# Kernel tuning notes

Measured on AMD Instinct MI355X. Metric: run time of the kernel, lower is better.

Reference implementation:

```python
import jax, jax.numpy as jnp
import numpy as np

N, E, H, B = 100000, 1600000, 64, 256
EPS = 1e-5


def ln(x, g, b):
    mu = jnp.mean(x, axis=-1, keepdims=True)
    var = jnp.mean((x - mu) ** 2, axis=-1, keepdims=True)
    return (x - mu) * jax.lax.rsqrt(var + EPS) * g + b


def gelu(x):
    # torch nn.GELU default is exact (erf) gelu
    return jax.nn.gelu(x, approximate=False)


def setup_inputs() -> dict:
    key = jax.random.key(0)
    ks = iter(jax.random.split(key, 64))
    nk = lambda: next(ks)
    s = 0.1
    p = {}
    p["x"] = jax.random.normal(nk(), (N, 2), jnp.float32)
    p["edge_attr"] = jax.random.normal(nk(), (E, 2), jnp.float32)
    # node_embed: Linear(2,H) LN GELU Linear(H,H) LN GELU (dropout = eval no-op)
    p["ne_w1"] = jax.random.normal(nk(), (2, H), jnp.float32) * s
    p["ne_b1"] = jnp.zeros((H,), jnp.float32)
    p["ne_g1"] = jnp.ones((H,), jnp.float32)
    p["ne_be1"] = jnp.zeros((H,), jnp.float32)
    p["ne_w2"] = jax.random.normal(nk(), (H, H), jnp.float32) * s
    p["ne_b2"] = jnp.zeros((H,), jnp.float32)
    p["ne_g2"] = jnp.ones((H,), jnp.float32)
    p["ne_be2"] = jnp.zeros((H,), jnp.float32)
    # 3 TrackConv layers: message MLP Linear(H+2,H)+LN, conv output LN, and outer per-layer LN
    p["conv_w"] = jax.random.normal(nk(), (3, H + 2, H), jnp.float32) * s
    p["conv_b"] = jnp.zeros((3, H), jnp.float32)
    p["conv_mg"] = jnp.ones((3, H), jnp.float32)
    p["conv_mb"] = jnp.zeros((3, H), jnp.float32)
    p["conv_ng"] = jnp.ones((3, H), jnp.float32)
    p["conv_nb"] = jnp.zeros((3, H), jnp.float32)
    p["out_ng"] = jnp.ones((3, H), jnp.float32)
    p["out_nb"] = jnp.zeros((3, H), jnp.float32)
    # head MLP: Linear(H,H)+LN+ReLU, Linear(H,H//2)+LN+ReLU, Linear(H//2,1)
    p["m_w1"] = jax.random.normal(nk(), (H, H), jnp.float32) * s
    p["m_b1"] = jnp.zeros((H,), jnp.float32)
    p["m_g1"] = jnp.ones((H,), jnp.float32)
    p["m_be1"] = jnp.zeros((H,), jnp.float32)
    p["m_w2"] = jax.random.normal(nk(), (H, H // 2), jnp.float32) * s
    p["m_b2"] = jnp.zeros((H // 2,), jnp.float32)
    p["m_g2"] = jnp.ones((H // 2,), jnp.float32)
    p["m_be2"] = jnp.zeros((H // 2,), jnp.float32)
    p["m_w3"] = jax.random.normal(nk(), (H // 2, 1), jnp.float32) * s
    p["m_b3"] = jnp.zeros((1,), jnp.float32)
    p["edge_index"] = jax.random.randint(nk(), (2, E), 0, N, dtype=jnp.int32)
    p["batch"] = jnp.sort(jax.random.randint(nk(), (N,), 0, B, dtype=jnp.int32))
    return p


def reference(x, edge_attr,
              ne_w1, ne_b1, ne_g1, ne_be1, ne_w2, ne_b2, ne_g2, ne_be2,
              conv_w, conv_b, conv_mg, conv_mb, conv_ng, conv_nb, out_ng, out_nb,
              m_w1, m_b1, m_g1, m_be1, m_w2, m_b2, m_g2, m_be2, m_w3, m_b3,
              edge_index, batch):
    # node embedding (dropout in eval = identity)
    h = gelu(ln(x @ ne_w1 + ne_b1, ne_g1, ne_be1))
    h = gelu(ln(h @ ne_w2 + ne_b2, ne_g2, ne_be2))
    src, dst = edge_index[0], edge_index[1]  # PyG: message from src (x_j), aggregate at dst
    deg = jax.ops.segment_sum(jnp.ones((E,), h.dtype), dst, num_segments=N)
    deg = jnp.maximum(deg, 1.0)[:, None]
    for l in range(3):
        msg_in = jnp.concatenate([h[src], edge_attr], axis=-1)  # [E, H+2]
        msg = gelu(ln(msg_in @ conv_w[l] + conv_b[l], conv_mg[l], conv_mb[l]))  # [E, H]
        agg = jax.ops.segment_sum(msg, dst, num_segments=N) / deg  # mean aggregate
        conv_out = ln(agg + h, conv_ng[l], conv_nb[l])  # TrackConv: norm(out + residual)
        h = h + ln(conv_out, out_ng[l], out_nb[l])  # outer norm + residual
    # global mean pool over graphs
    cnt = jnp.maximum(jax.ops.segment_sum(jnp.ones((N,), h.dtype), batch, num_segments=B), 1.0)[:, None]
    g = jax.ops.segment_sum(h, batch, num_segments=B) / cnt  # [B, H]
    g = jax.nn.relu(ln(g @ m_w1 + m_b1, m_g1, m_be1))
    g = jax.nn.relu(ln(g @ m_w2 + m_b2, m_g2, m_be2))
    return g @ m_w3 + m_b3  # [B, 1]
```

## Files before the change

kernel.cpp:

```cpp
#include <hip/hip_runtime.h>
#include <math.h>


typedef __attribute__((ext_vector_type(8))) short bfrag;
typedef __attribute__((ext_vector_type(4))) float ffrag;

template <int CTRL>
__device__ __forceinline__ float dpp_mov(float v) {
  return __int_as_float(
      __builtin_amdgcn_update_dpp(0, __float_as_int(v), CTRL, 0xF, 0xF, true));
}

__device__ __forceinline__ float rsum16(float v) {
  v += dpp_mov<0x128>(v);
  v += dpp_mov<0x124>(v);
  v += dpp_mov<0x122>(v);
  v += dpp_mov<0x121>(v);
  return v;
}

__device__ __forceinline__ float wave_sum64(float v) {
  v = rsum16(v);
  v += __shfl_xor(v, 16, 64);
  v += __shfl_xor(v, 32, 64);
  return v;
}

__device__ __forceinline__ float ln_apply(float t, float g, float b) {
  float s1 = wave_sum64(t);
  float s2 = wave_sum64(t * t);
  float mu = s1 * 0.015625f;
  float var = fmaf(-mu, mu, s2 * 0.015625f);
  return (t - mu) * rsqrtf(var + 1e-5f) * g + b;
}

__device__ __forceinline__ float erf_fast(float x) {
  float ax = fabsf(x);
  float p = fmaf(fmaf(fmaf(fmaf(0.078108f, ax, 0.000972f), ax, 0.230389f),
                      ax, 0.278393f), ax, 1.0f);
  p = p * p;
  p = p * p;
  float r = __builtin_amdgcn_rcpf(p);
  return copysignf(1.0f - r, x);
}

__device__ __forceinline__ float gelu_exact(float v) {
  float half = 0.5f * v;
  return fmaf(half, erf_fast(v * 0.70710678118654752440f), half);
}

__device__ __forceinline__ float lane_bcast(float v, int k) {
  return __uint_as_float(__builtin_amdgcn_readlane(__float_as_uint(v), k));
}

__device__ __forceinline__ short f2bf(float f) {
  union { float f; unsigned u; } v; v.f = f;
  unsigned r = v.u + 0x7fffu + ((v.u >> 16) & 1u);
  return (short)(r >> 16);
}

__global__ __launch_bounds__(256) void k_init1(
    const float* __restrict__ conv_w, ushort* __restrict__ wt,
    const int* __restrict__ ei, int* __restrict__ csr,
    int ne, int oHist) {
  const int bid = blockIdx.x;
  const int tid = threadIdx.x;
  if (bid < oHist) {
    const int i = bid * 256 + tid;
    const int k = i % 96, f = (i / 96) % 64, l = i / (96 * 64);
    const float v = (k < 66) ? conv_w[(size_t)l * 66 * 64 + k * 64 + f] : 0.0f;
    wt[i] = (ushort)f2bf(v);
    return;
  }
  const int i = (bid - oHist) * 256 + tid;
  if (i < ne) atomicAdd(&csr[__builtin_nontemporal_load(ei + ne + i)], 1);
}

__global__ __launch_bounds__(1024) void k_scan_fast(int* __restrict__ buf, int n) {
  __shared__ int wsum[16];
  const int tid = threadIdx.x, lane = tid & 63, w = tid >> 6;
  const int chunk = (((n + 1023) / 1024) + 3) & ~3;
  const int a = min(tid * chunk, n), b = min(a + chunk, n);
  const bool full = (a + chunk <= n);
  int s = 0;
  if (full) {
    const int4* p4 = (const int4*)(buf + a);
#pragma unroll 4
    for (int i = 0; i < chunk / 4; i++) {
      int4 v = p4[i];
      s += v.x + v.y + v.z + v.w;
    }
  } else {
    for (int i = a; i < b; i++) s += buf[i];
  }
  int inc = s;
#pragma unroll
  for (int sh = 1; sh < 64; sh <<= 1) {
    int t = __shfl_up(inc, sh, 64);
    if (lane >= sh) inc += t;
  }
  if (lane == 63) wsum[w] = inc;
  __syncthreads();
  int wb = 0;
  for (int j = 0; j < w; j++) wb += wsum[j];
  int excl = wb + inc - s;
  if (full) {
    int4* p4 = (int4*)(buf + a);
#pragma unroll 4
    for (int i = 0; i < chunk / 4; i++) {
      int4 v = p4[i];
      int4 o;
      o.x = excl; excl += v.x;
      o.y = excl; excl += v.y;
      o.z = excl; excl += v.z;
      o.w = excl; excl += v.w;
      p4[i] = o;
    }
  } else {
    for (int i = a; i < b; i++) { int v = buf[i]; buf[i] = excl; excl += v; }
  }
}

__global__ __launch_bounds__(256) void k_combo(
    const int* __restrict__ ei, const float* __restrict__ ea,
    int* __restrict__ cursor, int4* __restrict__ edata,
    const float* __restrict__ x,
    const float* __restrict__ w1, const float* __restrict__ b1,
    const float* __restrict__ g1, const float* __restrict__ be1,
    const float* __restrict__ w2, const float* __restrict__ b2,
    const float* __restrict__ g2, const float* __restrict__ be2,
    float* __restrict__ h, ushort* __restrict__ hb,
    int n_nodes, int ne, int nOrd, int embWaves, float roleScale) {
  const int bid = blockIdx.x;
  const int tid = threadIdx.x;
  const int sub = bid & 31;
  if (sub < 24) {
    const int role = bid & 7;
    const int ord = (bid >> 5) * 3 + (sub >> 3);
    const int lo = (int)((long long)ord * ne / nOrd);
    const int hi = (int)((long long)(ord + 1) * ne / nOrd);
    for (int i = lo + tid; i < hi; i += 256) {
      const int d = __builtin_nontemporal_load(ei + ne + i);
      const int rd = min(7, (int)((float)d * roleScale));
      if (rd == role) {
        const int s = __builtin_nontemporal_load(ei + i);
        const unsigned long long eau =
            __builtin_nontemporal_load((const unsigned long long*)ea + i);
        const float e0 = __uint_as_float((unsigned)eau);
        const float e1 = __uint_as_float((unsigned)(eau >> 32));
        const unsigned pk = (unsigned)(ushort)f2bf(e0) |
                            ((unsigned)(ushort)f2bf(e1) << 16);
        const int pos = atomicAdd(&cursor[d], 1);
        edata[pos] = make_int4(s, (int)pk, d, 0);
      }
    }
    return;
  }
  const int lane = tid & 63;
  const int eblk = (bid >> 5) * 8 + (sub - 24);
  const int wid = (eblk * 256 + tid) >> 6;
  const int nw = embWaves;
  float wc[64];
#pragma unroll
  for (int k = 0; k < 64; k++) wc[k] = w2[k * 64 + lane];
  const float w1a = w1[lane], w1b = w1[64 + lane];
  const float vb1 = b1[lane], vg1 = g1[lane], vbe1 = be1[lane];
  const float vb2 = b2[lane], vg2 = g2[lane], vbe2 = be2[lane];
  for (int n = wid; n < n_nodes; n += nw) {
    const float x0 = x[2 * n], x1 = x[2 * n + 1];
    float t = fmaf(x0, w1a, fmaf(x1, w1b, vb1));
    t = gelu_exact(ln_apply(t, vg1, vbe1));
    float a0 = vb2, a1 = 0.f, a2 = 0.f, a3 = 0.f;
#pragma unroll
    for (int k = 0; k < 64; k += 4) {
      a0 = fmaf(lane_bcast(t, k + 0), wc[k + 0], a0);
      a1 = fmaf(lane_bcast(t, k + 1), wc[k + 1], a1);
      a2 = fmaf(lane_bcast(t, k + 2), wc[k + 2], a2);
      a3 = fmaf(lane_bcast(t, k + 3), wc[k + 3], a3);
    }
    float acc = (a0 + a1) + (a2 + a3);
    acc = gelu_exact(ln_apply(acc, vg2, vbe2));
    __builtin_nontemporal_store(acc, h + (size_t)n * 64 + lane);
    __builtin_nontemporal_store((ushort)f2bf(acc),
                                hb + (size_t)n * 64 + lane);
  }
}

__global__ __launch_bounds__(256, 3) void k_edge_packed(
    const ushort* __restrict__ hb_in, float* __restrict__ agg,
    const int4* __restrict__ edata, const ushort* __restrict__ wt,
    const float* __restrict__ bias, const float* __restrict__ mg,
    const float* __restrict__ mb, int nchunks, int ne) {
  __shared__ __align__(16) ushort lwt[64 * 96];
  {
    const uint4* s = (const uint4*)wt;
    uint4* d = (uint4*)lwt;
    for (int i = threadIdx.x; i < 768; i += 256) d[i] = s[i];
  }
  __syncthreads();

  const int lane = threadIdx.x & 63;
  const int grp = lane >> 4, col = lane & 15;
  const int wid = (blockIdx.x * blockDim.x + threadIdx.x) >> 6;
  const int nw = (gridDim.x * blockDim.x) >> 6;

  float vb[4], vg[4], vbb[4];
#pragma unroll
  for (int t = 0; t < 4; t++) {
    const int f = t * 16 + col;
    vb[t] = bias[f]; vg[t] = mg[f]; vbb[t] = mb[f];
  }

  int c = wid;
  if (c >= nchunks) return;
  int4 e = edata[min(16 * c + col, ne - 1)];
  const ushort* hp0 = hb_in + (size_t)e.x * 64 + grp * 8;
  bfrag A0 = *(const bfrag*)(hp0);
  bfrag A1 = *(const bfrag*)(hp0 + 32);

  for (;;) {
    const int rem = min(16, ne - 16 * c);
    const int cn = c + nw;
    const bool more = cn < nchunks;
    const int nslot = more ? min(16 * cn + col, ne - 1) : min(16 * c + col, ne - 1);
    const int4 en = edata[nslot];

    bfrag A2 = {0, 0, 0, 0, 0, 0, 0, 0};
    if (grp == 0) {
      A2[0] = (short)(e.y & 0xffff);
      A2[1] = (short)((unsigned)e.y >> 16);
    }

    ffrag acc[4];
#pragma unroll
    for (int t = 0; t < 4; t++) { ffrag cc = {vb[t], vb[t], vb[t], vb[t]}; acc[t] = cc; }
#pragma unroll
    for (int t = 0; t < 4; t++) {
      const bfrag B = *(const bfrag*)(lwt + (t * 16 + col) * 96 + grp * 8);
      acc[t] = __builtin_amdgcn_mfma_f32_16x16x32_bf16(A0, B, acc[t], 0, 0, 0);
    }
#pragma unroll
    for (int t = 0; t < 4; t++) {
      const bfrag B = *(const bfrag*)(lwt + (t * 16 + col) * 96 + 32 + grp * 8);
      acc[t] = __builtin_amdgcn_mfma_f32_16x16x32_bf16(A1, B, acc[t], 0, 0, 0);
    }
#pragma unroll
    for (int t = 0; t < 4; t++) {
      const bfrag B = *(const bfrag*)(lwt + (t * 16 + col) * 96 + 64 + grp * 8);
      acc[t] = __builtin_amdgcn_mfma_f32_16x16x32_bf16(A2, B, acc[t], 0, 0, 0);
    }

    const ushort* hq = hb_in + (size_t)en.x * 64 + grp * 8;
    const bfrag N0 = *(const bfrag*)(hq);
    const bfrag N1 = *(const bfrag*)(hq + 32);

    float sx[4], sq[4];
#pragma unroll
    for (int r = 0; r < 4; r++) {
      float s = (acc[0][r] + acc[1][r]) + (acc[2][r] + acc[3][r]);
      float q = fmaf(acc[0][r], acc[0][r], fmaf(acc[1][r], acc[1][r],
                fmaf(acc[2][r], acc[2][r], acc[3][r] * acc[3][r])));
      sx[r] = s; sq[r] = q;
    }
#pragma unroll
    for (int r = 0; r < 4; r++) sx[r] = rsum16(sx[r]);
#pragma unroll
    for (int r = 0; r < 4; r++) sq[r] = rsum16(sq[r]);
    float iv[4], mi[4];
#pragma unroll
    for (int r = 0; r < 4; r++) {
      const float mu = sx[r] * 0.015625f;
      const float var = fmaf(-mu, mu, sq[r] * 0.015625f);
      iv[r] = rsqrtf(var + 1e-5f);
      mi[r] = -mu * iv[r];
    }

#pragma unroll
    for (int t = 0; t < 4; t++) {
#pragma unroll
      for (int r = 0; r < 4; r++) {
        const float z = fmaf(acc[t][r], iv[r], mi[r]);
        acc[t][r] = gelu_exact(fmaf(z, vg[t], vbb[t]));
      }
    }

    const int prev = __shfl_up(e.z, 1, 64);
    const unsigned long long bal = __ballot((col > 0) && (e.z != prev));
    const unsigned bm = (unsigned)bal & 0xFFFEu;

    int s0 = 0;
    while (s0 < rem) {
      const unsigned rest = bm >> (s0 + 1);
      int s1 = rest ? (s0 + 1 + __builtin_ctz(rest)) : 16;
      if (s1 > rem) s1 = rem;
      const int dseg = __builtin_amdgcn_readlane(e.z, s0);
#pragma unroll
      for (int t = 0; t < 4; t++) {
        float rs = 0.f;
#pragma unroll
        for (int r = 0; r < 4; r++) {
          const int row = grp * 4 + r;
          const float w = (row >= s0 && row < s1) ? 1.0f : 0.0f;
          rs = fmaf(acc[t][r], w, rs);
        }
        rs += __shfl_xor(rs, 16, 64);
        rs += __shfl_xor(rs, 32, 64);
        if (lane < 16)
          atomicAdd(&agg[(size_t)dseg * 64 + t * 16 + lane], rs);
      }
      s0 = s1;
    }

    if (!more) break;
    c = cn; e = en; A0 = N0; A1 = N1;
  }
}

__global__ void k_node_update(float* __restrict__ h, ushort* __restrict__ hb,
                              float* __restrict__ agg, const int* __restrict__ ends,
                              const float* __restrict__ ng, const float* __restrict__ nb,
                              const float* __restrict__ og, const float* __restrict__ ob,
                              int n_nodes, int writeHb) {
  const int lane = threadIdx.x & 63;
  const int n = (blockIdx.x * blockDim.x + threadIdx.x) >> 6;
  if (n >= n_nodes) return;
  int start, end;
  if (n == 0) { start = 0; end = ends[0]; }
  else { const int2 se = *(const int2*)(ends + n - 1); start = se.x; end = se.y; }
  const float dg = fmaxf((float)(end - start), 1.0f);
  const float hv = h[(size_t)n * 64 + lane];
  const float a = agg[(size_t)n * 64 + lane] / dg + hv;
  if (writeHb) agg[(size_t)n * 64 + lane] = 0.0f;
  const float c = ln_apply(a, ng[lane], nb[lane]);
  const float o = ln_apply(c, og[lane], ob[lane]);
  const float outv = hv + o;
  h[(size_t)n * 64 + lane] = outv;
  if (writeHb) hb[(size_t)n * 64 + lane] = (ushort)f2bf(outv);
}

__global__ void k_pool_seg(const float* __restrict__ h, const int* __restrict__ batch,
                           float* __restrict__ g, float* __restrict__ cnt,
                           int n_nodes, int chunk) {
  const int lane = threadIdx.x & 63;
  const int wid = (blockIdx.x * blockDim.x + threadIdx.x) >> 6;
  const int n0 = wid * chunk;
  if (n0 >= n_nodes) return;
  const int n1 = min(n0 + chunk, n_nodes);
  int cur = batch[n0], c = 0;
  float acc = 0.f;
  for (int n = n0; n < n1; n++) {
    const int b = batch[n];
    if (b != cur) {
      atomicAdd(&g[(size_t)cur * 64 + lane], acc);
      if (lane == 0) atomicAdd(&cnt[cur], (float)c);
      acc = 0.f; c = 0; cur = b;
    }
    acc += h[(size_t)n * 64 + lane];
    c++;
  }
  atomicAdd(&g[(size_t)cur * 64 + lane], acc);
  if (lane == 0) atomicAdd(&cnt[cur], (float)c);
}

__global__ void k_head(const float* __restrict__ g, const float* __restrict__ cnt,
                       const float* __restrict__ w1, const float* __restrict__ b1,
                       const float* __restrict__ g1, const float* __restrict__ be1,
                       const float* __restrict__ w2, const float* __restrict__ b2,
                       const float* __restrict__ g2, const float* __restrict__ be2,
                       const float* __restrict__ w3, const float* __restrict__ b3,
                       float* __restrict__ out, int nb_) {
  const int lane = threadIdx.x & 63;
  const int row = (blockIdx.x * blockDim.x + threadIdx.x) >> 6;
  if (row >= nb_) return;
  const float c = fmaxf(cnt[row], 1.0f);
  const float gv = g[row * 64 + lane] / c;
  float a0 = b1[lane], a1 = 0.f, a2 = 0.f, a3 = 0.f;
#pragma unroll
  for (int k = 0; k < 64; k += 4) {
    a0 = fmaf(lane_bcast(gv, k + 0), w1[(k + 0) * 64 + lane], a0);
    a1 = fmaf(lane_bcast(gv, k + 1), w1[(k + 1) * 64 + lane], a1);
    a2 = fmaf(lane_bcast(gv, k + 2), w1[(k + 2) * 64 + lane], a2);
    a3 = fmaf(lane_bcast(gv, k + 3), w1[(k + 3) * 64 + lane], a3);
  }
  float t = (a0 + a1) + (a2 + a3);
  t = fmaxf(ln_apply(t, g1[lane], be1[lane]), 0.0f);

  const int j = lane & 31;
  float c0 = b2[j], c1 = 0.f, c2 = 0.f, c3 = 0.f;
#pragma unroll
  for (int k = 0; k < 64; k += 4) {
    c0 = fmaf(lane_bcast(t, k + 0), w2[(k + 0) * 32 + j], c0);
    c1 = fmaf(lane_bcast(t, k + 1), w2[(k + 1) * 32 + j], c1);
    c2 = fmaf(lane_bcast(t, k + 2), w2[(k + 2) * 32 + j], c2);
    c3 = fmaf(lane_bcast(t, k + 3), w2[(k + 3) * 32 + j], c3);
  }
  float t2 = (c0 + c1) + (c2 + c3);
  t2 = fmaxf(ln_apply(t2, g2[j], be2[j]), 0.0f);
  const float p = t2 * w3[j];
  const float s = wave_sum64(p) * 0.5f;
  if (lane == 0) out[row] = s + b3[0];
}

extern "C" void kernel_launch(void* const* d_in, const int* in_sizes, int n_in,
                              void* d_out, int out_size, void* d_ws, size_t ws_size,
                              hipStream_t stream) {
  const float* x      = (const float*)d_in[0];
  const float* ea     = (const float*)d_in[1];
  const float* ne_w1  = (const float*)d_in[2];
  const float* ne_b1  = (const float*)d_in[3];
  const float* ne_g1  = (const float*)d_in[4];
  const float* ne_be1 = (const float*)d_in[5];
  const float* ne_w2  = (const float*)d_in[6];
  const float* ne_b2  = (const float*)d_in[7];
  const float* ne_g2  = (const float*)d_in[8];
  const float* ne_be2 = (const float*)d_in[9];
  const float* conv_w = (const float*)d_in[10];
  const float* conv_b = (const float*)d_in[11];
  const float* conv_mg= (const float*)d_in[12];
  const float* conv_mb= (const float*)d_in[13];
  const float* conv_ng= (const float*)d_in[14];
  const float* conv_nb= (const float*)d_in[15];
  const float* out_ng = (const float*)d_in[16];
  const float* out_nb = (const float*)d_in[17];
  const float* m_w1   = (const float*)d_in[18];
  const float* m_b1   = (const float*)d_in[19];
  const float* m_g1   = (const float*)d_in[20];
  const float* m_be1  = (const float*)d_in[21];
  const float* m_w2   = (const float*)d_in[22];
  const float* m_b2   = (const float*)d_in[23];
  const float* m_g2   = (const float*)d_in[24];
  const float* m_be2  = (const float*)d_in[25];
  const float* m_w3   = (const float*)d_in[26];
  const float* m_b3   = (const float*)d_in[27];
  const int*   eidx   = (const int*)d_in[28];
  const int*   batch  = (const int*)d_in[29];
  float* outp = (float*)d_out;

  const int NN = in_sizes[29];
  const int NE = in_sizes[1] / 2;
  const int NB = out_size;
  const int NCH = (NE + 15) / 16;

  char* wsb = (char*)d_ws;
  float*  h    = (float*)wsb;
  ushort* hb   = (ushort*)(h + (size_t)NN * 64);
  int4*   edata= (int4*)((char*)hb + ((size_t)NN * 128 + 15) / 16 * 16);
  ushort* wt   = (ushort*)(edata + NE);
  float*  gbuf = (float*)(wt + 3 * 64 * 96);
  float*  cnt  = gbuf + (size_t)NB * 64;
  int*    csr  = (int*)(cnt + NB);
  float*  agg  = (float*)((char*)(csr + NN) +
                          (((size_t)(uintptr_t)(csr + NN) & 15) ? 16 - ((size_t)(uintptr_t)(csr + NN) & 15) : 0));

  const dim3 blk(256);

  const size_t zbytes = (char*)(agg + (size_t)NN * 64) - (char*)gbuf;
  hipMemsetAsync(gbuf, 0, zbytes, stream);

  const int nPrep = (3 * 64 * 96) / 256;
  const int nHist = (NE + 255) / 256;
  k_init1<<<nPrep + nHist, blk, 0, stream>>>(conv_w, wt, eidx, csr, NE, nPrep);

  k_scan_fast<<<1, 1024, 0, stream>>>(csr, NN);

  const int ngroups = 261;
  const int nOrd = ngroups * 3;
  const int nEmb = ngroups * 8;
  k_combo<<<ngroups * 32, blk, 0, stream>>>(
      eidx, ea, csr, edata, x,
      ne_w1, ne_b1, ne_g1, ne_be1, ne_w2, ne_b2, ne_g2, ne_be2,
      h, hb, NN, NE, nOrd, nEmb * 4, 8.0f / (float)NN);

  for (int l = 0; l < 3; l++) {
    k_edge_packed<<<4096, blk, 0, stream>>>(
        hb, agg, edata, wt + (size_t)l * 64 * 96,
        conv_b + l * 64, conv_mg + l * 64, conv_mb + l * 64, NCH, NE);
    k_node_update<<<(NN * 64 + 255) / 256, blk, 0, stream>>>(
        h, hb, agg, csr, conv_ng + l * 64, conv_nb + l * 64,
        out_ng + l * 64, out_nb + l * 64, NN, (l < 2) ? 1 : 0);
  }

  {
    const int chunk = 32;
    const int nwaves = (NN + chunk - 1) / chunk;
    const int nblocks = (nwaves * 64 + 255) / 256;
    k_pool_seg<<<nblocks, blk, 0, stream>>>(h, batch, gbuf, cnt, NN, chunk);
  }
  k_head<<<(NB + 3) / 4, blk, 0, stream>>>(gbuf, cnt, m_w1, m_b1, m_g1, m_be1,
                                           m_w2, m_b2, m_g2, m_be2, m_w3, m_b3,
                                           outp, NB);
}
```

Measured before the change: 744.6 us.

## Bucket edges by destination block and aggregate messages in LDS before storing

Edges are now sorted only into buckets of 131 destination nodes rather than fully by destination. Each record is packed into an int2 holding the source index, the local destination offset and the bf16 edge attributes. The edge kernel runs one block per bucket and accumulates messages with LDS atomics into a padded local tile, then writes the tile to global agg with plain stores. This removes global float atomics, the per-node agg zeroing, and half of the edge-record bandwidth. In exchange, per-bucket work can be uneven, LDS atomic contention rises, and LDS use per block grows, which may lower occupancy.

```diff
diff --git a/kernel.cpp b/kernel.cpp
--- a/kernel.cpp
+++ b/kernel.cpp
@@ -4,6 +4,11 @@
 
 typedef __attribute__((ext_vector_type(8))) short bfrag;
 typedef __attribute__((ext_vector_type(4))) float ffrag;
+typedef __attribute__((ext_vector_type(4))) float f32x4;
+
+#define WBUK 131
+#define MAGW 4196609267u
+#define LSTR 68
 
 template <int CTRL>
 __device__ __forceinline__ float dpp_mov(float v) {
@@ -76,7 +81,9 @@
   if (i < ne) atomicAdd(&csr[__builtin_nontemporal_load(ei + ne + i)], 1);
 }
 
-__global__ __launch_bounds__(1024) void k_scan_fast(int* __restrict__ buf, int n) {
+__global__ __launch_bounds__(1024) void k_scan_fast(int* __restrict__ buf,
+                                                    int* __restrict__ bcur,
+                                                    int n, int nbuck) {
   __shared__ int wsum[16];
   const int tid = threadIdx.x, lane = tid & 63, w = tid >> 6;
   const int chunk = (((n + 1023) / 1024) + 3) & ~3;
@@ -119,18 +126,26 @@
   } else {
     for (int i = a; i < b; i++) { int v = buf[i]; buf[i] = excl; excl += v; }
   }
+  __syncthreads();
+  if (tid == 0) {
+    int tot = 0;
+#pragma unroll
+    for (int j = 0; j < 16; j++) tot += wsum[j];
+    buf[n] = tot;
+  }
+  for (int bq = tid; bq < nbuck; bq += 1024) bcur[bq] = buf[min(bq * WBUK, n)];
 }
 
 __global__ __launch_bounds__(256) void k_combo(
     const int* __restrict__ ei, const float* __restrict__ ea,
-    int* __restrict__ cursor, int4* __restrict__ edata,
+    int* __restrict__ bcur, int2* __restrict__ edata,
     const float* __restrict__ x,
     const float* __restrict__ w1, const float* __restrict__ b1,
     const float* __restrict__ g1, const float* __restrict__ be1,
     const float* __restrict__ w2, const float* __restrict__ b2,
     const float* __restrict__ g2, const float* __restrict__ be2,
     float* __restrict__ h, ushort* __restrict__ hb,
-    int n_nodes, int ne, int nOrd, int embWaves, float roleScale) {
+    int n_nodes, int ne, int nOrd, int embWaves) {
   const int bid = blockIdx.x;
   const int tid = threadIdx.x;
   const int sub = bid & 31;
@@ -141,8 +156,8 @@
     const int hi = (int)((long long)(ord + 1) * ne / nOrd);
     for (int i = lo + tid; i < hi; i += 256) {
       const int d = __builtin_nontemporal_load(ei + ne + i);
-      const int rd = min(7, (int)((float)d * roleScale));
-      if (rd == role) {
+      const unsigned bq = __umulhi((unsigned)d, MAGW) >> 7;
+      if ((int)(bq & 7u) == role) {
         const int s = __builtin_nontemporal_load(ei + i);
         const unsigned long long eau =
             __builtin_nontemporal_load((const unsigned long long*)ea + i);
@@ -150,8 +165,9 @@
         const float e1 = __uint_as_float((unsigned)(eau >> 32));
         const unsigned pk = (unsigned)(ushort)f2bf(e0) |
                             ((unsigned)(ushort)f2bf(e1) << 16);
-        const int pos = atomicAdd(&cursor[d], 1);
-        edata[pos] = make_int4(s, (int)pk, d, 0);
+        const int dloc = d - (int)bq * WBUK;
+        const int pos = atomicAdd(&bcur[bq], 1);
+        edata[pos] = make_int2(s | (dloc << 20), (int)pk);
       }
     }
     return;
@@ -186,23 +202,31 @@
   }
 }
 
-__global__ __launch_bounds__(256, 3) void k_edge_packed(
+__global__ __launch_bounds__(256, 3) void k_edge_lds(
     const ushort* __restrict__ hb_in, float* __restrict__ agg,
-    const int4* __restrict__ edata, const ushort* __restrict__ wt,
+    const int2* __restrict__ edata, const int* __restrict__ csr,
+    const ushort* __restrict__ wt,
     const float* __restrict__ bias, const float* __restrict__ mg,
-    const float* __restrict__ mb, int nchunks, int ne) {
+    const float* __restrict__ mb, int nn) {
   __shared__ __align__(16) ushort lwt[64 * 96];
+  __shared__ __align__(16) float lagg[WBUK * LSTR];
   {
     const uint4* s = (const uint4*)wt;
     uint4* d = (uint4*)lwt;
     for (int i = threadIdx.x; i < 768; i += 256) d[i] = s[i];
-  }
+    f32x4* z = (f32x4*)lagg;
+    const f32x4 zz = {0.f, 0.f, 0.f, 0.f};
+    for (int i = threadIdx.x; i < (WBUK * LSTR) / 4; i += 256) z[i] = zz;
+  }
+  const int bq = blockIdx.x;
+  const int nlo = bq * WBUK;
+  const int nhi = min(nlo + WBUK, nn);
+  const int lo = csr[nlo], hi = csr[nhi];
   __syncthreads();
 
   const int lane = threadIdx.x & 63;
+  const int wv = threadIdx.x >> 6;
   const int grp = lane >> 4, col = lane & 15;
-  const int wid = (blockIdx.x * blockDim.x + threadIdx.x) >> 6;
-  const int nw = (gridDim.x * blockDim.x) >> 6;
 
   float vb[4], vg[4], vbb[4];
 #pragma unroll
@@ -211,126 +235,122 @@
     vb[t] = bias[f]; vg[t] = mg[f]; vbb[t] = mb[f];
   }
 
-  int c = wid;
-  if (c >= nchunks) return;
-  int4 e = edata[min(16 * c + col, ne - 1)];
-  const ushort* hp0 = hb_in + (size_t)e.x * 64 + grp * 8;
-  bfrag A0 = *(const bfrag*)(hp0);
-  bfrag A1 = *(const bfrag*)(hp0 + 32);
-
-  for (;;) {
-    const int rem = min(16, ne - 16 * c);
-    const int cn = c + nw;
-    const bool more = cn < nchunks;
-    const int nslot = more ? min(16 * cn + col, ne - 1) : min(16 * c + col, ne - 1);
-    const int4 en = edata[nslot];
-
-    bfrag A2 = {0, 0, 0, 0, 0, 0, 0, 0};
-    if (grp == 0) {
-      A2[0] = (short)(e.y & 0xffff);
-      A2[1] = (short)((unsigned)e.y >> 16);
+  const int nch = (hi - lo + 15) >> 4;
+  int c = wv;
+  if (c < nch) {
+    int slot = min(lo + 16 * c + col, hi - 1);
+    int2 e = edata[slot];
+    const ushort* hp0 = hb_in + (size_t)(e.x & 0xFFFFF) * 64 + grp * 8;
+    bfrag A0 = *(const bfrag*)(hp0);
+    bfrag A1 = *(const bfrag*)(hp0 + 32);
+
+    for (;;) {
+      const int rem = min(16, hi - lo - 16 * c);
+      const int cn = c + 4;
+      const bool more = cn < nch;
+      const int nslot = more ? min(lo + 16 * cn + col, hi - 1) : slot;
+      const int2 en = edata[nslot];
+
+      bfrag A2 = {0, 0, 0, 0, 0, 0, 0, 0};
+      if (grp == 0) {
+        A2[0] = (short)(e.y & 0xffff);
+        A2[1] = (short)((unsigned)e.y >> 16);
+      }
+
+      ffrag acc[4];
+#pragma unroll
+      for (int t = 0; t < 4; t++) { ffrag cc = {vb[t], vb[t], vb[t], vb[t]}; acc[t] = cc; }
+#pragma unroll
+      for (int t = 0; t < 4; t++) {
+        const bfrag B = *(const bfrag*)(lwt + (t * 16 + col) * 96 + grp * 8);
+        acc[t] = __builtin_amdgcn_mfma_f32_16x16x32_bf16(A0, B, acc[t], 0, 0, 0);
+      }
+#pragma unroll
+      for (int t = 0; t < 4; t++) {
+        const bfrag B = *(const bfrag*)(lwt + (t * 16 + col) * 96 + 32 + grp * 8);
+        acc[t] = __builtin_amdgcn_mfma_f32_16x16x32_bf16(A1, B, acc[t], 0, 0, 0);
+      }
+#pragma unroll
+      for (int t = 0; t < 4; t++) {
+        const bfrag B = *(const bfrag*)(lwt + (t * 16 + col) * 96 + 64 + grp * 8);
+        acc[t] = __builtin_amdgcn_mfma_f32_16x16x32_bf16(A2, B, acc[t], 0, 0, 0);
+      }
+
+      const ushort* hq = hb_in + (size_t)(en.x & 0xFFFFF) * 64 + grp * 8;
+      const bfrag N0 = *(const bfrag*)(hq);
+      const bfrag N1 = *(const bfrag*)(hq + 32);
+
+      float sx[4], sq[4];
+#pragma unroll
+      for (int r = 0; r < 4; r++) {
+        float s = (acc[0][r] + acc[1][r]) + (acc[2][r] + acc[3][r]);
+        float q = fmaf(acc[0][r], acc[0][r], fmaf(acc[1][r], acc[1][r],
+                  fmaf(acc[2][r], acc[2][r], acc[3][r] * acc[3][r])));
+        sx[r] = s; sq[r] = q;
+      }
+#pragma unroll
+      for (int r = 0; r < 4; r++) sx[r] = rsum16(sx[r]);
+#pragma unroll
+      for (int r = 0; r < 4; r++) sq[r] = rsum16(sq[r]);
+      float iv[4], mi[4];
+#pragma unroll
+      for (int r = 0; r < 4; r++) {
+        const float mu = sx[r] * 0.015625f;
+        const float var = fmaf(-mu, mu, sq[r] * 0.015625f);
+        iv[r] = rsqrtf(var + 1e-5f);
+        mi[r] = -mu * iv[r];
+      }
+
+#pragma unroll
+      for (int t = 0; t < 4; t++) {
+#pragma unroll
+        for (int r = 0; r < 4; r++) {
+          const float z = fmaf(acc[t][r], iv[r], mi[r]);
+          acc[t][r] = gelu_exact(fmaf(z, vg[t], vbb[t]));
+        }
+      }
+
+      const int dloc = (int)(((unsigned)e.x) >> 20);
+      int ad[4];
+#pragma unroll
+      for (int r = 0; r < 4; r++)
+        ad[r] = __shfl(dloc, grp * 4 + r, 64) * LSTR;
+#pragma unroll
+      for (int r = 0; r < 4; r++) {
+        const int row = grp * 4 + r;
+        if (row < rem) {
+#pragma unroll
+          for (int t = 0; t < 4; t++)
+            atomicAdd(&lagg[ad[r] + t * 16 + col], acc[t][r]);
+        }
+      }
+
+      if (!more) break;
+      c = cn; slot = nslot; e = en; A0 = N0; A1 = N1;
     }
-
-    ffrag acc[4];
-#pragma unroll
-    for (int t = 0; t < 4; t++) { ffrag cc = {vb[t], vb[t], vb[t], vb[t]}; acc[t] = cc; }
-#pragma unroll
-    for (int t = 0; t < 4; t++) {
-      const bfrag B = *(const bfrag*)(lwt + (t * 16 + col) * 96 + grp * 8);
-      acc[t] = __builtin_amdgcn_mfma_f32_16x16x32_bf16(A0, B, acc[t], 0, 0, 0);
-    }
-#pragma unroll
-    for (int t = 0; t < 4; t++) {
-      const bfrag B = *(const bfrag*)(lwt + (t * 16 + col) * 96 + 32 + grp * 8);
-      acc[t] = __builtin_amdgcn_mfma_f32_16x16x32_bf16(A1, B, acc[t], 0, 0, 0);
-    }
-#pragma unroll
-    for (int t = 0; t < 4; t++) {
-      const bfrag B = *(const bfrag*)(lwt + (t * 16 + col) * 96 + 64 + grp * 8);
-      acc[t] = __builtin_amdgcn_mfma_f32_16x16x32_bf16(A2, B, acc[t], 0, 0, 0);
-    }
-
-    const ushort* hq = hb_in + (size_t)en.x * 64 + grp * 8;
-    const bfrag N0 = *(const bfrag*)(hq);
-    const bfrag N1 = *(const bfrag*)(hq + 32);
-
-    float sx[4], sq[4];
-#pragma unroll
-    for (int r = 0; r < 4; r++) {
-      float s = (acc[0][r] + acc[1][r]) + (acc[2][r] + acc[3][r]);
-      float q = fmaf(acc[0][r], acc[0][r], fmaf(acc[1][r], acc[1][r],
-                fmaf(acc[2][r], acc[2][r], acc[3][r] * acc[3][r])));
-      sx[r] = s; sq[r] = q;
-    }
-#pragma unroll
-    for (int r = 0; r < 4; r++) sx[r] = rsum16(sx[r]);
-#pragma unroll
-    for (int r = 0; r < 4; r++) sq[r] = rsum16(sq[r]);
-    float iv[4], mi[4];
-#pragma unroll
-    for (int r = 0; r < 4; r++) {
-      const float mu = sx[r] * 0.015625f;
-      const float var = fmaf(-mu, mu, sq[r] * 0.015625f);
-      iv[r] = rsqrtf(var + 1e-5f);
-      mi[r] = -mu * iv[r];
-    }
-
-#pragma unroll
-    for (int t = 0; t < 4; t++) {
-#pragma unroll
-      for (int r = 0; r < 4; r++) {
-        const float z = fmaf(acc[t][r], iv[r], mi[r]);
-        acc[t][r] = gelu_exact(fmaf(z, vg[t], vbb[t]));
-      }
-    }
-
-    const int prev = __shfl_up(e.z, 1, 64);
-    const unsigned long long bal = __ballot((col > 0) && (e.z != prev));
-    const unsigned bm = (unsigned)bal & 0xFFFEu;
-
-    int s0 = 0;
-    while (s0 < rem) {
-      const unsigned rest = bm >> (s0 + 1);
-      int s1 = rest ? (s0 + 1 + __builtin_ctz(rest)) : 16;
-      if (s1 > rem) s1 = rem;
-      const int dseg = __builtin_amdgcn_readlane(e.z, s0);
-#pragma unroll
-      for (int t = 0; t < 4; t++) {
-        float rs = 0.f;
-#pragma unroll
-        for (int r = 0; r < 4; r++) {
-          const int row = grp * 4 + r;
-          const float w = (row >= s0 && row < s1) ? 1.0f : 0.0f;
-          rs = fmaf(acc[t][r], w, rs);
-        }
-        rs += __shfl_xor(rs, 16, 64);
-        rs += __shfl_xor(rs, 32, 64);
-        if (lane < 16)
-          atomicAdd(&agg[(size_t)dseg * 64 + t * 16 + lane], rs);
-      }
-      s0 = s1;
-    }
-
-    if (!more) break;
-    c = cn; e = en; A0 = N0; A1 = N1;
+  }
+  __syncthreads();
+
+  const int wbk = nhi - nlo;
+  for (int u = threadIdx.x; u < wbk * 16; u += 256) {
+    const int i = u >> 4, j = u & 15;
+    const f32x4 v = *(const f32x4*)(lagg + i * LSTR + j * 4);
+    __builtin_nontemporal_store(v, (f32x4*)(agg + ((size_t)(nlo + i) * 64 + j * 4)));
   }
 }
 
 __global__ void k_node_update(float* __restrict__ h, ushort* __restrict__ hb,
-                              float* __restrict__ agg, const int* __restrict__ ends,
+                              const float* __restrict__ agg, const int* __restrict__ csr,
                               const float* __restrict__ ng, const float* __restrict__ nb,
                               const float* __restrict__ og, const float* __restrict__ ob,
                               int n_nodes, int writeHb) {
   const int lane = threadIdx.x & 63;
   const int n = (blockIdx.x * blockDim.x + threadIdx.x) >> 6;
   if (n >= n_nodes) return;
-  int start, end;
-  if (n == 0) { start = 0; end = ends[0]; }
-  else { const int2 se = *(const int2*)(ends + n - 1); start = se.x; end = se.y; }
-  const float dg = fmaxf((float)(end - start), 1.0f);
+  const int2 se = *(const int2*)(csr + n);
+  const float dg = fmaxf((float)(se.y - se.x), 1.0f);
   const float hv = h[(size_t)n * 64 + lane];
   const float a = agg[(size_t)n * 64 + lane] / dg + hv;
-  if (writeHb) agg[(size_t)n * 64 + lane] = 0.0f;
   const float c = ln_apply(a, ng[lane], nb[lane]);
   const float o = ln_apply(c, og[lane], ob[lane]);
   const float outv = hv + o;
@@ -439,42 +459,42 @@
   const int NN = in_sizes[29];
   const int NE = in_sizes[1] / 2;
   const int NB = out_size;
-  const int NCH = (NE + 15) / 16;
+  const int NBUCK = (NN + WBUK - 1) / WBUK;
 
   char* wsb = (char*)d_ws;
-  float*  h    = (float*)wsb;
-  ushort* hb   = (ushort*)(h + (size_t)NN * 64);
-  int4*   edata= (int4*)((char*)hb + ((size_t)NN * 128 + 15) / 16 * 16);
-  ushort* wt   = (ushort*)(edata + NE);
-  float*  gbuf = (float*)(wt + 3 * 64 * 96);
-  float*  cnt  = gbuf + (size_t)NB * 64;
-  int*    csr  = (int*)(cnt + NB);
-  float*  agg  = (float*)((char*)(csr + NN) +
-                          (((size_t)(uintptr_t)(csr + NN) & 15) ? 16 - ((size_t)(uintptr_t)(csr + NN) & 15) : 0));
+  float*  h     = (float*)wsb;
+  ushort* hb    = (ushort*)(h + (size_t)NN * 64);
+  int2*   edata = (int2*)((char*)hb + (size_t)NN * 128);
+  ushort* wt    = (ushort*)(edata + NE);
+  float*  agg   = (float*)(wt + 3 * 64 * 96);
+  float*  gbuf  = agg + (size_t)NN * 64;
+  float*  cnt   = gbuf + (size_t)NB * 64;
+  int*    csr   = (int*)(cnt + NB);
+  int*    bcur  = csr + (NN + 1);
 
   const dim3 blk(256);
 
-  const size_t zbytes = (char*)(agg + (size_t)NN * 64) - (char*)gbuf;
+  const size_t zbytes = (char*)(bcur + NBUCK) - (char*)gbuf;
   hipMemsetAsync(gbuf, 0, zbytes, stream);
 
   const int nPrep = (3 * 64 * 96) / 256;
   const int nHist = (NE + 255) / 256;
   k_init1<<<nPrep + nHist, blk, 0, stream>>>(conv_w, wt, eidx, csr, NE, nPrep);
 
-  k_scan_fast<<<1, 1024, 0, stream>>>(csr, NN);
+  k_scan_fast<<<1, 1024, 0, stream>>>(csr, bcur, NN, NBUCK);
 
   const int ngroups = 261;
   const int nOrd = ngroups * 3;
   const int nEmb = ngroups * 8;
   k_combo<<<ngroups * 32, blk, 0, stream>>>(
-      eidx, ea, csr, edata, x,
+      eidx, ea, bcur, edata, x,
       ne_w1, ne_b1, ne_g1, ne_be1, ne_w2, ne_b2, ne_g2, ne_be2,
-      h, hb, NN, NE, nOrd, nEmb * 4, 8.0f / (float)NN);
+      h, hb, NN, NE, nOrd, nEmb * 4);
 
   for (int l = 0; l < 3; l++) {
-    k_edge_packed<<<4096, blk, 0, stream>>>(
-        hb, agg, edata, wt + (size_t)l * 64 * 96,
-        conv_b + l * 64, conv_mg + l * 64, conv_mb + l * 64, NCH, NE);
+    k_edge_lds<<<NBUCK, blk, 0, stream>>>(
+        hb, agg, edata, csr, wt + (size_t)l * 64 * 96,
+        conv_b + l * 64, conv_mg + l * 64, conv_mb + l * 64, NN);
     k_node_update<<<(NN * 64 + 255) / 256, blk, 0, stream>>>(
         h, hb, agg, csr, conv_ng + l * 64, conv_nb + l * 64,
         out_ng + l * 64, out_nb + l * 64, NN, (l < 2) ? 1 : 0);
```

Result: slower. 2.530 ms (+239.8%).

## Fuse edge message and node update into per-wave destination-range layer kernel

Applied to the files above, without the earlier changes.

The scan kernel now also builds a balanced partition that gives each of 16384 waves a contiguous range of destination nodes holding roughly equal edge counts. A new fused layer kernel processes the sorted edges of its node range, keeps per-segment partial sums in registers and applies the mean, both LayerNorms and the residual in place. This removes the global agg buffer, its float atomics, the zeroing and the separate node-update launch. The bf16 features are double-buffered so that in-place updates cannot corrupt neighbours still being read. The cost is possible load imbalance from high-degree nodes, plus serial handling of nodes with no edges.

```diff
diff --git a/kernel.cpp b/kernel.cpp
--- a/kernel.cpp
+++ b/kernel.cpp
@@ -4,6 +4,8 @@
 
 typedef __attribute__((ext_vector_type(8))) short bfrag;
 typedef __attribute__((ext_vector_type(4))) float ffrag;
+
+#define NWV 16384
 
 template <int CTRL>
 __device__ __forceinline__ float dpp_mov(float v) {
@@ -76,7 +78,9 @@
   if (i < ne) atomicAdd(&csr[__builtin_nontemporal_load(ei + ne + i)], 1);
 }
 
-__global__ __launch_bounds__(1024) void k_scan_fast(int* __restrict__ buf, int n) {
+__global__ __launch_bounds__(1024) void k_scan_fast(int* __restrict__ buf,
+                                                    int* __restrict__ wstart,
+                                                    int n, int nwv) {
   __shared__ int wsum[16];
   const int tid = threadIdx.x, lane = tid & 63, w = tid >> 6;
   const int chunk = (((n + 1023) / 1024) + 3) & ~3;
@@ -103,22 +107,42 @@
   __syncthreads();
   int wb = 0;
   for (int j = 0; j < w; j++) wb += wsum[j];
+  int total = 0;
+#pragma unroll
+  for (int j = 0; j < 16; j++) total += wsum[j];
   int excl = wb + inc - s;
+
+#define EMITW(idx, st, en)                                                    \
+  {                                                                           \
+    if ((en) > (st)) {                                                        \
+      int wlo = (int)(((long long)(st) * nwv + total - 1) / total);           \
+      int whi = (int)(((long long)(en) * nwv + total - 1) / total);           \
+      for (int ww = wlo; ww < whi; ww++) wstart[ww] = (idx);                  \
+    }                                                                         \
+  }
+
   if (full) {
     int4* p4 = (int4*)(buf + a);
 #pragma unroll 4
     for (int i = 0; i < chunk / 4; i++) {
       int4 v = p4[i];
       int4 o;
-      o.x = excl; excl += v.x;
-      o.y = excl; excl += v.y;
-      o.z = excl; excl += v.z;
-      o.w = excl; excl += v.w;
+      o.x = excl; EMITW(a + i * 4 + 0, excl, excl + v.x); excl += v.x;
+      o.y = excl; EMITW(a + i * 4 + 1, excl, excl + v.y); excl += v.y;
+      o.z = excl; EMITW(a + i * 4 + 2, excl, excl + v.z); excl += v.z;
+      o.w = excl; EMITW(a + i * 4 + 3, excl, excl + v.w); excl += v.w;
       p4[i] = o;
     }
   } else {
-    for (int i = a; i < b; i++) { int v = buf[i]; buf[i] = excl; excl += v; }
-  }
+    for (int i = a; i < b; i++) {
+      int v = buf[i];
+      buf[i] = excl;
+      EMITW(i, excl, excl + v);
+      excl += v;
+    }
+  }
+#undef EMITW
+  if (tid == 0) wstart[nwv] = n;
 }
 
 __global__ __launch_bounds__(256) void k_combo(
@@ -186,11 +210,30 @@
   }
 }
 
-__global__ __launch_bounds__(256, 3) void k_edge_packed(
-    const ushort* __restrict__ hb_in, float* __restrict__ agg,
-    const int4* __restrict__ edata, const ushort* __restrict__ wt,
+__device__ __forceinline__ void node_finish(
+    float tot, float dgf, float hv, int d, int lane,
+    float ngv, float nbv, float ogv, float obv,
+    float* __restrict__ h, ushort* __restrict__ hb_out, int writeHb) {
+  const float a = tot / dgf + hv;
+  const float c = ln_apply(a, ngv, nbv);
+  const float o = ln_apply(c, ogv, obv);
+  const float outv = hv + o;
+  __builtin_nontemporal_store(outv, h + (size_t)d * 64 + lane);
+  if (writeHb)
+    __builtin_nontemporal_store((ushort)f2bf(outv),
+                                hb_out + (size_t)d * 64 + lane);
+}
+
+__global__ __launch_bounds__(256, 3) void k_layer(
+    const ushort* __restrict__ hb_in, ushort* __restrict__ hb_out,
+    float* __restrict__ h,
+    const int4* __restrict__ edata, const int* __restrict__ csr,
+    const int* __restrict__ wstart, const ushort* __restrict__ wt,
     const float* __restrict__ bias, const float* __restrict__ mg,
-    const float* __restrict__ mb, int nchunks, int ne) {
+    const float* __restrict__ mb,
+    const float* __restrict__ ng, const float* __restrict__ nb,
+    const float* __restrict__ og, const float* __restrict__ ob,
+    int writeHb) {
   __shared__ __align__(16) ushort lwt[64 * 96];
   {
     const uint4* s = (const uint4*)wt;
@@ -200,9 +243,15 @@
   __syncthreads();
 
   const int lane = threadIdx.x & 63;
+  const int wgl = (int)((blockIdx.x * blockDim.x + threadIdx.x) >> 6);
+  const int n0 = wstart[wgl], n1 = wstart[wgl + 1];
+  if (n0 >= n1) return;
+  const int e_lo = (n0 > 0) ? csr[n0 - 1] : 0;
+  const int e_hi = csr[n1 - 1];
+
   const int grp = lane >> 4, col = lane & 15;
-  const int wid = (blockIdx.x * blockDim.x + threadIdx.x) >> 6;
-  const int nw = (gridDim.x * blockDim.x) >> 6;
+  const float ngv = ng[lane], nbv = nb[lane];
+  const float ogv = og[lane], obv = ob[lane];
 
   float vb[4], vg[4], vbb[4];
 #pragma unroll
@@ -211,131 +260,150 @@
     vb[t] = bias[f]; vg[t] = mg[f]; vbb[t] = mb[f];
   }
 
-  int c = wid;
-  if (c >= nchunks) return;
-  int4 e = edata[min(16 * c + col, ne - 1)];
-  const ushort* hp0 = hb_in + (size_t)e.x * 64 + grp * 8;
-  bfrag A0 = *(const bfrag*)(hp0);
-  bfrag A1 = *(const bfrag*)(hp0 + 32);
-
-  for (;;) {
-    const int rem = min(16, ne - 16 * c);
-    const int cn = c + nw;
-    const bool more = cn < nchunks;
-    const int nslot = more ? min(16 * cn + col, ne - 1) : min(16 * c + col, ne - 1);
-    const int4 en = edata[nslot];
-
-    bfrag A2 = {0, 0, 0, 0, 0, 0, 0, 0};
-    if (grp == 0) {
-      A2[0] = (short)(e.y & 0xffff);
-      A2[1] = (short)((unsigned)e.y >> 16);
-    }
-
-    ffrag acc[4];
-#pragma unroll
-    for (int t = 0; t < 4; t++) { ffrag cc = {vb[t], vb[t], vb[t], vb[t]}; acc[t] = cc; }
-#pragma unroll
-    for (int t = 0; t < 4; t++) {
-      const bfrag B = *(const bfrag*)(lwt + (t * 16 + col) * 96 + grp * 8);
-      acc[t] = __builtin_amdgcn_mfma_f32_16x16x32_bf16(A0, B, acc[t], 0, 0, 0);
-    }
-#pragma unroll
-    for (int t = 0; t < 4; t++) {
-      const bfrag B = *(const bfrag*)(lwt + (t * 16 + col) * 96 + 32 + grp * 8);
-      acc[t] = __builtin_amdgcn_mfma_f32_16x16x32_bf16(A1, B, acc[t], 0, 0, 0);
-    }
-#pragma unroll
-    for (int t = 0; t < 4; t++) {
-      const bfrag B = *(const bfrag*)(lwt + (t * 16 + col) * 96 + 64 + grp * 8);
-      acc[t] = __builtin_amdgcn_mfma_f32_16x16x32_bf16(A2, B, acc[t], 0, 0, 0);
-    }
-
-    const ushort* hq = hb_in + (size_t)en.x * 64 + grp * 8;
-    const bfrag N0 = *(const bfrag*)(hq);
-    const bfrag N1 = *(const bfrag*)(hq + 32);
-
-    float sx[4], sq[4];
-#pragma unroll
-    for (int r = 0; r < 4; r++) {
-      float s = (acc[0][r] + acc[1][r]) + (acc[2][r] + acc[3][r]);
-      float q = fmaf(acc[0][r], acc[0][r], fmaf(acc[1][r], acc[1][r],
-                fmaf(acc[2][r], acc[2][r], acc[3][r] * acc[3][r])));
-      sx[r] = s; sq[r] = q;
-    }
-#pragma unroll
-    for (int r = 0; r < 4; r++) sx[r] = rsum16(sx[r]);
-#pragma unroll
-    for (int r = 0; r < 4; r++) sq[r] = rsum16(sq[r]);
-    float iv[4], mi[4];
-#pragma unroll
-    for (int r = 0; r < 4; r++) {
-      const float mu = sx[r] * 0.015625f;
-      const float var = fmaf(-mu, mu, sq[r] * 0.015625f);
-      iv[r] = rsqrtf(var + 1e-5f);
-      mi[r] = -mu * iv[r];
-    }
-
-#pragma unroll
-    for (int t = 0; t < 4; t++) {
+  int nextn = n0;
+  int nstart = e_lo;
+  float car[4] = {0.f, 0.f, 0.f, 0.f};
+
+  const int nch = (e_hi - e_lo + 15) >> 4;
+  if (nch > 0) {
+    int slot = min(e_lo + col, e_hi - 1);
+    int4 e = edata[slot];
+    const ushort* hp0 = hb_in + (size_t)e.x * 64 + grp * 8;
+    bfrag A0 = *(const bfrag*)(hp0);
+    bfrag A1 = *(const bfrag*)(hp0 + 32);
+
+    for (int c = 0;;) {
+      const int rem = min(16, e_hi - e_lo - 16 * c);
+      const bool more = (c + 1) < nch;
+      const int nslot = more ? min(e_lo + 16 * (c + 1) + col, e_hi - 1) : slot;
+      const int4 en = edata[nslot];
+
+      const int d0t = __builtin_amdgcn_readlane(e.z, 0);
+      const float hpre = h[(size_t)d0t * 64 + lane];
+
+      bfrag A2 = {0, 0, 0, 0, 0, 0, 0, 0};
+      if (grp == 0) {
+        A2[0] = (short)(e.y & 0xffff);
+        A2[1] = (short)((unsigned)e.y >> 16);
+      }
+
+      ffrag acc[4];
+#pragma unroll
+      for (int t = 0; t < 4; t++) { ffrag cc = {vb[t], vb[t], vb[t], vb[t]}; acc[t] = cc; }
+#pragma unroll
+      for (int t = 0; t < 4; t++) {
+        const bfrag B = *(const bfrag*)(lwt + (t * 16 + col) * 96 + grp * 8);
+        acc[t] = __builtin_amdgcn_mfma_f32_16x16x32_bf16(A0, B, acc[t], 0, 0, 0);
+      }
+#pragma unroll
+      for (int t = 0; t < 4; t++) {
+        const bfrag B = *(const bfrag*)(lwt + (t * 16 + col) * 96 + 32 + grp * 8);
+        acc[t] = __builtin_amdgcn_mfma_f32_16x16x32_bf16(A1, B, acc[t], 0, 0, 0);
+      }
+#pragma unroll
+      for (int t = 0; t < 4; t++) {
+        const bfrag B = *(const bfrag*)(lwt + (t * 16 + col) * 96 + 64 + grp * 8);
+        acc[t] = __builtin_amdgcn_mfma_f32_16x16x32_bf16(A2, B, acc[t], 0, 0, 0);
+      }
+
+      const ushort* hq = hb_in + (size_t)en.x * 64 + grp * 8;
+      const bfrag N0 = *(const bfrag*)(hq);
+      const bfrag N1 = *(const bfrag*)(hq + 32);
+
+      float sx[4], sq[4];
 #pragma unroll
       for (int r = 0; r < 4; r++) {
-        const float z = fmaf(acc[t][r], iv[r], mi[r]);
-        acc[t][r] = gelu_exact(fmaf(z, vg[t], vbb[t]));
-      }
-    }
-
-    const int prev = __shfl_up(e.z, 1, 64);
-    const unsigned long long bal = __ballot((col > 0) && (e.z != prev));
-    const unsigned bm = (unsigned)bal & 0xFFFEu;
-
-    int s0 = 0;
-    while (s0 < rem) {
-      const unsigned rest = bm >> (s0 + 1);
-      int s1 = rest ? (s0 + 1 + __builtin_ctz(rest)) : 16;
-      if (s1 > rem) s1 = rem;
-      const int dseg = __builtin_amdgcn_readlane(e.z, s0);
+        float s = (acc[0][r] + acc[1][r]) + (acc[2][r] + acc[3][r]);
+        float q = fmaf(acc[0][r], acc[0][r], fmaf(acc[1][r], acc[1][r],
+                  fmaf(acc[2][r], acc[2][r], acc[3][r] * acc[3][r])));
+        sx[r] = s; sq[r] = q;
+      }
+#pragma unroll
+      for (int r = 0; r < 4; r++) sx[r] = rsum16(sx[r]);
+#pragma unroll
+      for (int r = 0; r < 4; r++) sq[r] = rsum16(sq[r]);
+      float iv[4], mi[4];
+#pragma unroll
+      for (int r = 0; r < 4; r++) {
+        const float mu = sx[r] * 0.015625f;
+        const float var = fmaf(-mu, mu, sq[r] * 0.015625f);
+        iv[r] = rsqrtf(var + 1e-5f);
+        mi[r] = -mu * iv[r];
+      }
+
 #pragma unroll
       for (int t = 0; t < 4; t++) {
-        float rs = 0.f;
 #pragma unroll
         for (int r = 0; r < 4; r++) {
-          const int row = grp * 4 + r;
-          const float w = (row >= s0 && row < s1) ? 1.0f : 0.0f;
-          rs = fmaf(acc[t][r], w, rs);
+          const float z = fmaf(acc[t][r], iv[r], mi[r]);
+          acc[t][r] = gelu_exact(fmaf(z, vg[t], vbb[t]));
         }
-        rs += __shfl_xor(rs, 16, 64);
-        rs += __shfl_xor(rs, 32, 64);
-        if (lane < 16)
-          atomicAdd(&agg[(size_t)dseg * 64 + t * 16 + lane], rs);
-      }
-      s0 = s1;
-    }
-
-    if (!more) break;
-    c = cn; e = en; A0 = N0; A1 = N1;
-  }
-}
-
-__global__ void k_node_update(float* __restrict__ h, ushort* __restrict__ hb,
-                              float* __restrict__ agg, const int* __restrict__ ends,
-                              const float* __restrict__ ng, const float* __restrict__ nb,
-                              const float* __restrict__ og, const float* __restrict__ ob,
-                              int n_nodes, int writeHb) {
-  const int lane = threadIdx.x & 63;
-  const int n = (blockIdx.x * blockDim.x + threadIdx.x) >> 6;
-  if (n >= n_nodes) return;
-  int start, end;
-  if (n == 0) { start = 0; end = ends[0]; }
-  else { const int2 se = *(const int2*)(ends + n - 1); start = se.x; end = se.y; }
-  const float dg = fmaxf((float)(end - start), 1.0f);
-  const float hv = h[(size_t)n * 64 + lane];
-  const float a = agg[(size_t)n * 64 + lane] / dg + hv;
-  if (writeHb) agg[(size_t)n * 64 + lane] = 0.0f;
-  const float c = ln_apply(a, ng[lane], nb[lane]);
-  const float o = ln_apply(c, og[lane], ob[lane]);
-  const float outv = hv + o;
-  h[(size_t)n * 64 + lane] = outv;
-  if (writeHb) hb[(size_t)n * 64 + lane] = (ushort)f2bf(outv);
+      }
+
+      const int prev = __shfl_up(e.z, 1, 64);
+      const unsigned long long bal = __ballot((col > 0) && (e.z != prev));
+      const unsigned bm = (unsigned)bal & 0xFFFEu;
+      const int peek = more ? __builtin_amdgcn_readlane(en.z, 0) : -1;
+
+      int s0 = 0;
+      while (s0 < rem) {
+        const unsigned rest = bm >> (s0 + 1);
+        int s1 = rest ? (s0 + 1 + __builtin_ctz(rest)) : 16;
+        if (s1 > rem) s1 = rem;
+        const int dseg = __builtin_amdgcn_readlane(e.z, s0);
+
+        float rs[4];
+#pragma unroll
+        for (int t = 0; t < 4; t++) {
+          float r_ = 0.f;
+#pragma unroll
+          for (int r = 0; r < 4; r++) {
+            const int row = grp * 4 + r;
+            const float w = (row >= s0 && row < s1) ? 1.0f : 0.0f;
+            r_ = fmaf(acc[t][r], w, r_);
+          }
+          r_ += __shfl_xor(r_, 16, 64);
+          r_ += __shfl_xor(r_, 32, 64);
+          rs[t] = r_;
+        }
+
+        const bool comp = (s1 < rem) || (!more) || (peek != dseg);
+        if (comp) {
+          for (int n = nextn; n < dseg; n++) {
+            const float hv0 = h[(size_t)n * 64 + lane];
+            node_finish(0.f, 1.f, hv0, n, lane, ngv, nbv, ogv, obv,
+                        h, hb_out, writeHb);
+          }
+          const float t0 = __shfl(car[0] + rs[0], lane & 15, 64);
+          const float t1 = __shfl(car[1] + rs[1], lane & 15, 64);
+          const float t2 = __shfl(car[2] + rs[2], lane & 15, 64);
+          const float t3 = __shfl(car[3] + rs[3], lane & 15, 64);
+          const float tot = (lane < 16) ? t0 : (lane < 32) ? t1
+                              : (lane < 48) ? t2 : t3;
+          const int glob = e_lo + 16 * c + s1;
+          const float dgf = (float)(glob - nstart);
+          const float hv = (dseg == d0t) ? hpre : h[(size_t)dseg * 64 + lane];
+          node_finish(tot, dgf, hv, dseg, lane, ngv, nbv, ogv, obv,
+                      h, hb_out, writeHb);
+          car[0] = car[1] = car[2] = car[3] = 0.f;
+          nstart = glob;
+          nextn = dseg + 1;
+        } else {
+#pragma unroll
+          for (int t = 0; t < 4; t++) car[t] += rs[t];
+        }
+        s0 = s1;
+      }
+
+      if (!more) break;
+      c++; slot = nslot; e = en; A0 = N0; A1 = N1;
+    }
+  }
+  for (int n = nextn; n < n1; n++) {
+    const float hv0 = h[(size_t)n * 64 + lane];
+    node_finish(0.f, 1.f, hv0, n, lane, ngv, nbv, ogv, obv,
+                h, hb_out, writeHb);
+  }
 }
 
 __global__ void k_pool_seg(const float* __restrict__ h, const int* __restrict__ batch,
@@ -439,29 +507,28 @@
   const int NN = in_sizes[29];
   const int NE = in_sizes[1] / 2;
   const int NB = out_size;
-  const int NCH = (NE + 15) / 16;
 
   char* wsb = (char*)d_ws;
-  float*  h    = (float*)wsb;
-  ushort* hb   = (ushort*)(h + (size_t)NN * 64);
-  int4*   edata= (int4*)((char*)hb + ((size_t)NN * 128 + 15) / 16 * 16);
-  ushort* wt   = (ushort*)(edata + NE);
-  float*  gbuf = (float*)(wt + 3 * 64 * 96);
-  float*  cnt  = gbuf + (size_t)NB * 64;
-  int*    csr  = (int*)(cnt + NB);
-  float*  agg  = (float*)((char*)(csr + NN) +
-                          (((size_t)(uintptr_t)(csr + NN) & 15) ? 16 - ((size_t)(uintptr_t)(csr + NN) & 15) : 0));
+  float*  h     = (float*)wsb;
+  ushort* hbA   = (ushort*)(h + (size_t)NN * 64);
+  ushort* hbB   = hbA + (size_t)NN * 64;
+  int4*   edata = (int4*)(hbB + (size_t)NN * 64);
+  ushort* wt    = (ushort*)(edata + NE);
+  int*    wstart= (int*)(wt + 3 * 64 * 96);
+  float*  gbuf  = (float*)(wstart + (NWV + 1));
+  float*  cnt   = gbuf + (size_t)NB * 64;
+  int*    csr   = (int*)(cnt + NB);
 
   const dim3 blk(256);
 
-  const size_t zbytes = (char*)(agg + (size_t)NN * 64) - (char*)gbuf;
+  const size_t zbytes = (char*)(csr + NN) - (char*)gbuf;
   hipMemsetAsync(gbuf, 0, zbytes, stream);
 
   const int nPrep = (3 * 64 * 96) / 256;
   const int nHist = (NE + 255) / 256;
   k_init1<<<nPrep + nHist, blk, 0, stream>>>(conv_w, wt, eidx, csr, NE, nPrep);
 
-  k_scan_fast<<<1, 1024, 0, stream>>>(csr, NN);
+  k_scan_fast<<<1, 1024, 0, stream>>>(csr, wstart, NN, NWV);
 
   const int ngroups = 261;
   const int nOrd = ngroups * 3;
@@ -469,15 +536,16 @@
   k_combo<<<ngroups * 32, blk, 0, stream>>>(
       eidx, ea, csr, edata, x,
       ne_w1, ne_b1, ne_g1, ne_be1, ne_w2, ne_b2, ne_g2, ne_be2,
-      h, hb, NN, NE, nOrd, nEmb * 4, 8.0f / (float)NN);
+      h, hbA, NN, NE, nOrd, nEmb * 4, 8.0f / (float)NN);
 
   for (int l = 0; l < 3; l++) {
-    k_edge_packed<<<4096, blk, 0, stream>>>(
-        hb, agg, edata, wt + (size_t)l * 64 * 96,
-        conv_b + l * 64, conv_mg + l * 64, conv_mb + l * 64, NCH, NE);
-    k_node_update<<<(NN * 64 + 255) / 256, blk, 0, stream>>>(
-        h, hb, agg, csr, conv_ng + l * 64, conv_nb + l * 64,
-        out_ng + l * 64, out_nb + l * 64, NN, (l < 2) ? 1 : 0);
+    const ushort* hin = (l == 1) ? hbB : hbA;
+    ushort* hout = (l == 0) ? hbB : hbA;
+    k_layer<<<NWV / 4, blk, 0, stream>>>(
+        hin, hout, h, edata, csr, wstart, wt + (size_t)l * 64 * 96,
+        conv_b + l * 64, conv_mg + l * 64, conv_mb + l * 64,
+        conv_ng + l * 64, conv_nb + l * 64,
+        out_ng + l * 64, out_nb + l * 64, (l < 2) ? 1 : 0);
   }
 
   {
```

New measurement: 862.9 us. +15.9%, slower.
